# Kernel tuning notes

Hardware: AMD Instinct MI355X
Metric: run time of the kernel (lower is better)

Reference implementation:

```python
import jax, jax.numpy as jnp
import numpy as np

NUM_THRESHOLDS = 200
N = 4_000_000
KEPS = 1e-07
EPS = 1e-06


def _make_thresholds(num_thresholds=NUM_THRESHOLDS):
    inner = [(i + 1) * 1.0 / (num_thresholds - 1) for i in range(num_thresholds - 2)]
    return jnp.asarray([0.0 - KEPS] + inner + [1.0 + KEPS], dtype=jnp.float32)


def setup_inputs() -> dict:
    key = jax.random.key(0)
    k1, k2 = jax.random.split(key)
    predictions = jax.random.uniform(k1, (N,), dtype=jnp.float32)  # in [0,1]
    labels = jax.random.randint(k2, (N,), 0, 2, dtype=jnp.int32)
    thresholds = _make_thresholds()
    return {"predictions": predictions, "labels": labels, "thresholds": thresholds}


def reference(predictions, labels, thresholds):
    # Confusion matrix at all thresholds: [T, N] broadcast compare, reduce over N.
    lab_pos = labels.astype(bool)  # [N]
    pred_pos = predictions[None, :] > thresholds[:, None]  # [T, N] bool
    lab_pos_b = jnp.broadcast_to(lab_pos[None, :], pred_pos.shape)
    tp = jnp.sum(jnp.logical_and(lab_pos_b, pred_pos), axis=1).astype(jnp.float32)
    fn = jnp.sum(jnp.logical_and(lab_pos_b, ~pred_pos), axis=1).astype(jnp.float32)
    fp = jnp.sum(jnp.logical_and(~lab_pos_b, pred_pos), axis=1).astype(jnp.float32)
    tn = jnp.sum(jnp.logical_and(~lab_pos_b, ~pred_pos), axis=1).astype(jnp.float32)
    # Trapezoidal AUC over (FPR, TPR)
    rec = (tp + EPS) / (tp + fn + EPS)          # y (TPR)
    fp_rate = fp / (fp + tn + EPS)              # x (FPR)
    x, y = fp_rate, rec
    auc = jnp.sum((x[:-1] - x[1:]) * (y[:-1] + y[1:]) * 0.5)
    return auc
```

## Files before the change

### kernel.cpp

```cpp
#include <hip/hip_runtime.h>

#define NTH    200
#define NBINS  201
#define NROWS  (2 * NBINS)
#define NBLKH  256
#define HTPB   1024
#define HWAVES 16

__global__ void __launch_bounds__(HTPB)
auroc_hist_kernel(const float* __restrict__ preds,
                  const int*   __restrict__ labels,
                  const float* __restrict__ thresholds,
                  unsigned int* __restrict__ part,
                  int n) {
    __shared__ float        s_th[NTH];
    __shared__ unsigned int s_hist[HWAVES][NBINS];

    const int t    = threadIdx.x;
    const int wave = t >> 6;

    for (int i = t; i < HWAVES * NBINS; i += HTPB)
        ((unsigned int*)s_hist)[i] = 0u;
    for (int i = t; i < NTH; i += HTPB)
        s_th[i] = thresholds[i];
    __syncthreads();

    unsigned int* my = s_hist[wave];

    const int gid    = blockIdx.x * HTPB + t;
    const int stride = gridDim.x * HTPB;
    const int n4     = n >> 2;
    const float4* p4 = (const float4*)preds;
    const int4*   l4 = (const int4*)labels;

    for (int i = gid; i < n4; i += stride) {
        float4 p = p4[i];
        int4   l = l4[i];
        float  pv[4] = {p.x, p.y, p.z, p.w};
        int    lv[4] = {l.x, l.y, l.z, l.w};
#pragma unroll
        for (int j = 0; j < 4; ++j) {
            float pp = pv[j];
            int k0 = (int)(pp * 199.0f);
            k0 = k0 > 198 ? 198 : k0;
            float ta = s_th[k0];
            float tb = s_th[k0 + 1];
            int g = k0 + ((ta < pp) ? ((tb < pp) ? 2 : 1) : 0);
            unsigned int add = 1u | ((unsigned int)(lv[j] != 0) << 16);
            atomicAdd(&my[g], add);
        }
    }
    for (int i = (n4 << 2) + gid; i < n; i += stride) {
        float pp = preds[i];
        int k0 = (int)(pp * 199.0f);
        k0 = k0 > 198 ? 198 : k0;
        float ta = s_th[k0];
        float tb = s_th[k0 + 1];
        int g = k0 + ((ta < pp) ? ((tb < pp) ? 2 : 1) : 0);
        unsigned int add = 1u | ((unsigned int)(labels[i] != 0) << 16);
        atomicAdd(&my[g], add);
    }
    __syncthreads();

    const int b = blockIdx.x;
    for (int i = t; i < NBINS; i += HTPB) {
        unsigned int v = 0u;
#pragma unroll
        for (int w = 0; w < HWAVES; ++w) v += s_hist[w][i];
        unsigned int pos = v >> 16;
        unsigned int neg = (v & 0xFFFFu) - pos;
        part[i * NBLKH + b]           = pos;
        part[(NBINS + i) * NBLKH + b] = neg;
    }
}

__global__ void __launch_bounds__(512)
auroc_finish_kernel(const unsigned int* __restrict__ part,
                    float* __restrict__ out) {
    __shared__ unsigned int s_row[NROWS];
    __shared__ unsigned int s_sufp[NBINS + 1], s_sufn[NBINS + 1];
    __shared__ float s_x[NTH], s_y[NTH];

    const int t = threadIdx.x;

    if (t < NROWS) {
        const uint4* row = (const uint4*)(part + t * NBLKH);
        unsigned int acc = 0u;
#pragma unroll 8
        for (int j = 0; j < NBLKH / 4; ++j) {
            uint4 v = row[j];
            acc += v.x + v.y + v.z + v.w;
        }
        s_row[t] = acc;
    }
    if (t == 0) { s_sufp[NBINS] = 0u; s_sufn[NBINS] = 0u; }
    __syncthreads();

    if (t < NBINS) {
        unsigned int sp = 0u, sn = 0u;
        for (int k = t; k < NBINS; ++k) {
            sp += s_row[k];
            sn += s_row[NBINS + k];
        }
        s_sufp[t] = sp;
        s_sufn[t] = sn;
    }
    __syncthreads();

    const float P   = (float)s_sufp[0];
    const float Nn  = (float)s_sufn[0];
    const float EPS = 1e-6f;

    if (t < NTH) {
        float tp = (float)s_sufp[t + 1];
        float fp = (float)s_sufn[t + 1];
        float fn = P - tp;
        float tn = Nn - fp;
        s_y[t] = (tp + EPS) / (tp + fn + EPS);
        s_x[t] = fp / (fp + tn + EPS);
    }
    __syncthreads();

    if (t == 0) {
        double auc = 0.0;
        for (int i = 0; i < NTH - 1; ++i)
            auc += (double)((s_x[i] - s_x[i + 1]) * (s_y[i] + s_y[i + 1]) * 0.5f);
        out[0] = (float)auc;
    }
}

extern "C" void kernel_launch(void* const* d_in, const int* in_sizes, int n_in,
                              void* d_out, int out_size, void* d_ws, size_t ws_size,
                              hipStream_t stream) {
    const float* preds      = (const float*)d_in[0];
    const int*   labels     = (const int*)d_in[1];
    const float* thresholds = (const float*)d_in[2];
    float*       out        = (float*)d_out;
    unsigned int* part      = (unsigned int*)d_ws;

    const int n = in_sizes[0];

    auroc_hist_kernel<<<NBLKH, HTPB, 0, stream>>>(preds, labels, thresholds,
                                                  part, n);
    auroc_finish_kernel<<<1, 512, 0, stream>>>(part, out);
}
```

Before: 101.0 us.

## Use more, smaller histogram blocks and add a parallel cross-block reduce kernel

The histogram grid changes from 256 blocks of 1024 threads to 1024 blocks of 256 threads, each block keeping 4 per-wave shared histograms instead of 16. The per-bin sum over blocks moves out of the single-block finish kernel into a new kernel that launches one block per row and reduces it with wave shuffles. This is meant to spread the partial-sum reduction across the GPU and improve occupancy of the histogram kernel. In exchange it adds a third kernel launch and writes four times as many partial counts to global memory. The hard-coded 4-wave sum and the 256-thread uint4 load depend on the new constants.

```diff
diff --git a/kernel.cpp b/kernel.cpp
--- a/kernel.cpp
+++ b/kernel.cpp
@@ -3,9 +3,9 @@
 #define NTH    200
 #define NBINS  201
 #define NROWS  (2 * NBINS)
-#define NBLKH  256
-#define HTPB   1024
-#define HWAVES 16
+#define NBLKH  1024
+#define HTPB   256
+#define HWAVES 4
 
 __global__ void __launch_bounds__(HTPB)
 auroc_hist_kernel(const float* __restrict__ preds,
@@ -64,9 +64,7 @@
 
     const int b = blockIdx.x;
     for (int i = t; i < NBINS; i += HTPB) {
-        unsigned int v = 0u;
-#pragma unroll
-        for (int w = 0; w < HWAVES; ++w) v += s_hist[w][i];
+        unsigned int v = s_hist[0][i] + s_hist[1][i] + s_hist[2][i] + s_hist[3][i];
         unsigned int pos = v >> 16;
         unsigned int neg = (v & 0xFFFFu) - pos;
         part[i * NBLKH + b]           = pos;
@@ -74,8 +72,29 @@
     }
 }
 
-__global__ void __launch_bounds__(512)
-auroc_finish_kernel(const unsigned int* __restrict__ part,
+__global__ void __launch_bounds__(256)
+auroc_reduce_kernel(const unsigned int* __restrict__ part,
+                    unsigned int* __restrict__ hist2) {
+    __shared__ unsigned int s_w[4];
+
+    const int t = threadIdx.x;
+    const int r = blockIdx.x;
+
+    uint4 v = ((const uint4*)(part + r * NBLKH))[t];
+    unsigned int acc = v.x + v.y + v.z + v.w;
+
+#pragma unroll
+    for (int off = 32; off >= 1; off >>= 1)
+        acc += __shfl_down(acc, off, 64);
+
+    if ((t & 63) == 0) s_w[t >> 6] = acc;
+    __syncthreads();
+
+    if (t == 0) hist2[r] = s_w[0] + s_w[1] + s_w[2] + s_w[3];
+}
+
+__global__ void __launch_bounds__(256)
+auroc_finish_kernel(const unsigned int* __restrict__ hist2,
                     float* __restrict__ out) {
     __shared__ unsigned int s_row[NROWS];
     __shared__ unsigned int s_sufp[NBINS + 1], s_sufn[NBINS + 1];
@@ -83,16 +102,7 @@
 
     const int t = threadIdx.x;
 
-    if (t < NROWS) {
-        const uint4* row = (const uint4*)(part + t * NBLKH);
-        unsigned int acc = 0u;
-#pragma unroll 8
-        for (int j = 0; j < NBLKH / 4; ++j) {
-            uint4 v = row[j];
-            acc += v.x + v.y + v.z + v.w;
-        }
-        s_row[t] = acc;
-    }
+    for (int i = t; i < NROWS; i += 256) s_row[i] = hist2[i];
     if (t == 0) { s_sufp[NBINS] = 0u; s_sufn[NBINS] = 0u; }
     __syncthreads();
 
@@ -137,10 +147,12 @@
     const float* thresholds = (const float*)d_in[2];
     float*       out        = (float*)d_out;
     unsigned int* part      = (unsigned int*)d_ws;
+    unsigned int* hist2     = part + NROWS * NBLKH;
 
     const int n = in_sizes[0];
 
     auroc_hist_kernel<<<NBLKH, HTPB, 0, stream>>>(preds, labels, thresholds,
                                                   part, n);
-    auroc_finish_kernel<<<1, 512, 0, stream>>>(part, out);
+    auroc_reduce_kernel<<<NROWS, 256, 0, stream>>>(part, hist2);
+    auroc_finish_kernel<<<1, 256, 0, stream>>>(hist2, out);
 }
```

After: 91.64 us. -9.2%, faster.
